# Kernel tuning notes

Measured on AMD Instinct MI355X. Metric: run time of the kernel, lower is better.

The kernel has to match this reference:

```python
import jax, jax.numpy as jnp
import numpy as np

SIZE = 11
SIGMA = 1.5
DEPTH = 1
C1 = (0.01 * DEPTH) ** 2
C2 = (0.03 * DEPTH) ** 2


def _fspecial_gauss(size, sigma):
    # mimics the MATLAB fspecial gaussian used by the torch module
    x, y = np.mgrid[-size // 2 + 1: size // 2 + 1, -size // 2 + 1: size // 2 + 1]
    g = np.exp(-((x ** 2 + y ** 2) / (2.0 * sigma ** 2)))
    g = g / g.sum()
    return jnp.asarray(g, dtype=jnp.float32)[None, None]  # [1,1,size,size]


def setup_inputs() -> dict:
    key = jax.random.key(0)
    k1, k2 = jax.random.split(key)
    N, C, H, W = 64, 1, 512, 512
    y_hat = jax.random.uniform(k1, (N, C, H, W), dtype=jnp.float32)
    y = jax.random.uniform(k2, (N, C, H, W), dtype=jnp.float32)
    window = _fspecial_gauss(SIZE, SIGMA)
    return {"y_hat": y_hat, "y": y, "window": window}


def _conv(x, w):
    # valid conv, stride 1, NCHW / OIHW
    return jax.lax.conv_general_dilated(
        x, w, window_strides=(1, 1), padding="VALID",
        dimension_numbers=("NCHW", "OIHW", "NCHW"))


def _ssim(y_hat, y, window):
    N = y_hat.shape[0]
    # single conv over the 5 stacked maps (y_hat, y, y_hat^2, y^2, y_hat*y)
    stacked = jnp.concatenate(
        [y_hat, y, y_hat * y_hat, y * y, y_hat * y], axis=0)
    conv = _conv(stacked, window)
    mu1, mu2, s11, s22, s12 = jnp.split(conv, 5, axis=0)
    mu1_sq = mu1 * mu1
    mu2_sq = mu2 * mu2
    mu1_mu2 = mu1 * mu2
    sigma1_sq = s11 - mu1_sq
    sigma2_sq = s22 - mu2_sq
    sigma12 = s12 - mu1_mu2
    score = ((2 * mu1_mu2 + C1) * (2 * sigma12 + C2)) / (
        (mu1_sq + mu2_sq + C1) * (sigma1_sq + sigma2_sq + C2))
    return jnp.mean(score)


def reference(y_hat, y, window):
    return _ssim(y_hat, y, window)
```

## Files before the change

kernel.cpp:

```cpp
#include <hip/hip_runtime.h>

#define KS 11
#define TBX 32
#define TBY 32
#define NROWS 42
#define HST 34
#define IMG 512
#define OUT_H 502
#define OUT_W 502
#define N_IMG 64
#define GXD 16
#define GYD 16
#define NBLK (GXD * GYD * N_IMG)

__global__ __launch_bounds__(256, 4) void ssim_main(
    const float* __restrict__ g_a, const float* __restrict__ g_b,
    const float* __restrict__ g_w, float* __restrict__ bsum)
{
  __shared__ float s_h[5][NROWS][HST];
  __shared__ float s_red[4];

  const int t = threadIdx.x;
  const int x0 = blockIdx.x * TBX, y0 = blockIdx.y * TBY;
  const float* __restrict__ A = g_a + (size_t)blockIdx.z * (IMG * IMG);
  const float* __restrict__ B = g_b + (size_t)blockIdx.z * (IMG * IMG);

  float u[KS];
  {
    const float inv = 1.0f / sqrtf(g_w[5 * KS + 5]);
#pragma unroll
    for (int j = 0; j < KS; ++j) u[j] = g_w[j * KS + 5] * inv;
  }

  const bool edge = (x0 == IMG - TBX) || (y0 == IMG - TBX);
  if (t < 252) {
    const int r = t / 6;
    const int k = t - r * 6;
    const int c0 = (k == 5) ? 26 : 6 * k;
    const int gy = y0 + r;
    const int gxs = x0 + c0;

    float ea[16], eb[16];
    if (!edge) {
      const float* pa = A + gy * IMG + gxs;
      const float* pb = B + gy * IMG + gxs;
#pragma unroll
      for (int i = 0; i < 8; ++i) {
        const float2 va = *(const float2*)(pa + 2 * i);
        const float2 vb = *(const float2*)(pb + 2 * i);
        ea[2 * i] = va.x; ea[2 * i + 1] = va.y;
        eb[2 * i] = vb.x; eb[2 * i + 1] = vb.y;
      }
    } else {
      const int gyc = min(gy, IMG - 1);
      const float* pa = A + gyc * IMG;
      const float* pb = B + gyc * IMG;
#pragma unroll
      for (int i = 0; i < 16; ++i) {
        const int gx = min(gxs + i, IMG - 1);
        ea[i] = pa[gx];
        eb[i] = pb[gx];
      }
    }

    float hm1[6], hm2[6], h11[6], h22[6], h12[6];
#pragma unroll
    for (int cc = 0; cc < 6; ++cc) {
      float m1 = 0.f, m2 = 0.f, q11 = 0.f, q22 = 0.f, q12 = 0.f;
#pragma unroll
      for (int j = 0; j < KS; ++j) {
        const float a = ea[cc + j], b = eb[cc + j];
        const float ta = u[j] * a, tb = u[j] * b;
        m1 += ta;
        m2 += tb;
        q11 = fmaf(ta, a, q11);
        q22 = fmaf(tb, b, q22);
        q12 = fmaf(ta, b, q12);
      }
      hm1[cc] = m1; hm2[cc] = m2; h11[cc] = q11; h22[cc] = q22; h12[cc] = q12;
    }

#define WRMAP(m, arr)                                                   \
    *(float2*)&s_h[m][r][c0]     = make_float2(arr[0], arr[1]);         \
    *(float2*)&s_h[m][r][c0 + 2] = make_float2(arr[2], arr[3]);         \
    *(float2*)&s_h[m][r][c0 + 4] = make_float2(arr[4], arr[5]);
    WRMAP(0, hm1) WRMAP(1, hm2) WRMAP(2, h11) WRMAP(3, h22) WRMAP(4, h12)
#undef WRMAP
  }
  __syncthreads();

  const int x = t & 31;
  const int yq = (t >> 5) << 2;
  float omu1[4], omu2[4], os11[4], os22[4], os12[4];

  auto vconv = [&](int m, float* o) {
    float v[14];
#pragma unroll
    for (int kk = 0; kk < 14; ++kk) v[kk] = s_h[m][yq + kk][x];
#pragma unroll
    for (int yy = 0; yy < 4; ++yy) {
      float a_ = 0.f;
#pragma unroll
      for (int i = 0; i < KS; ++i) a_ = fmaf(u[i], v[yy + i], a_);
      o[yy] = a_;
    }
  };
  vconv(0, omu1);
  vconv(1, omu2);
  vconv(2, os11);
  vconv(3, os22);
  vconv(4, os12);

  float score = 0.f;
  const int gx_ = x0 + x;
#pragma unroll
  for (int yy = 0; yy < 4; ++yy) {
    const int gy_ = y0 + yq + yy;
    if (gx_ < OUT_W && gy_ < OUT_H) {
      const float C1 = 1e-4f, C2 = 9e-4f;
      const float mu1 = omu1[yy], mu2 = omu2[yy];
      const float mu1s = mu1 * mu1, mu2s = mu2 * mu2, m12 = mu1 * mu2;
      const float sig1 = os11[yy] - mu1s, sig2 = os22[yy] - mu2s,
                  sig12 = os12[yy] - m12;
      score += ((2.f * m12 + C1) * (2.f * sig12 + C2)) /
               ((mu1s + mu2s + C1) * (sig1 + sig2 + C2));
    }
  }

#pragma unroll
  for (int off = 32; off > 0; off >>= 1)
    score += __shfl_down(score, off);
  const int wave = t >> 6, lane = t & 63;
  if (lane == 0) s_red[wave] = score;
  __syncthreads();
  if (t == 0) {
    const int bid = (int)((blockIdx.z * GYD + blockIdx.y) * GXD + blockIdx.x);
    bsum[bid] = s_red[0] + s_red[1] + s_red[2] + s_red[3];
  }
}

__global__ __launch_bounds__(256) void ssim_final(
    const float* __restrict__ bsum, float* __restrict__ out)
{
  double v = 0.0;
  for (int i = threadIdx.x; i < NBLK; i += 256) v += (double)bsum[i];
#pragma unroll
  for (int off = 32; off > 0; off >>= 1)
    v += __shfl_down(v, off);
  __shared__ double s_red[4];
  const int wave = (int)threadIdx.x >> 6, lane = (int)threadIdx.x & 63;
  if (lane == 0) s_red[wave] = v;
  __syncthreads();
  if (threadIdx.x == 0) {
    const double total = s_red[0] + s_red[1] + s_red[2] + s_red[3];
    out[0] = (float)(total / (double)((size_t)N_IMG * OUT_H * OUT_W));
  }
}

extern "C" void kernel_launch(void* const* d_in, const int* in_sizes, int n_in,
                              void* d_out, int out_size, void* d_ws, size_t ws_size,
                              hipStream_t stream) {
  const float* yh = (const float*)d_in[0];
  const float* yy = (const float*)d_in[1];
  const float* w  = (const float*)d_in[2];
  float* bsum = (float*)d_ws;
  float* out = (float*)d_out;

  dim3 grid(GXD, GYD, N_IMG);
  hipLaunchKernelGGL(ssim_main, grid, dim3(256), 0, stream, yh, yy, w, bsum);
  hipLaunchKernelGGL(ssim_final, dim3(1), dim3(256), 0, stream, bsum, out);
}
```

Before: 257.8 us.

## Use ring-buffered shared rows with two-phase separable SSIM to shrink LDS

Replaces the 42-row horizontal-pass buffer with a 32-slot ring buffer filled in two phases, so each block computes the first 16 output rows, refills 16 new rows and then computes the rest. This lowers LDS per block and raises the launch-bounds occupancy hint from 4 to 8 blocks. Horizontal tasks now cover 4 columns each with float4 loads, and the row stride changes to 35 to avoid bank conflicts. It adds an extra barrier pair and serialises two load/compute phases. The final reduction also reads the block sums with float4 loads.

```diff
diff --git a/kernel.cpp b/kernel.cpp
--- a/kernel.cpp
+++ b/kernel.cpp
@@ -3,8 +3,8 @@
 #define KS 11
 #define TBX 32
 #define TBY 32
-#define NROWS 42
-#define HST 34
+#define SLOTS 32
+#define HST 35
 #define IMG 512
 #define OUT_H 502
 #define OUT_W 502
@@ -12,18 +12,20 @@
 #define GXD 16
 #define GYD 16
 #define NBLK (GXD * GYD * N_IMG)
+#define MSTRIDE (SLOTS * HST)
 
-__global__ __launch_bounds__(256, 4) void ssim_main(
+__global__ __launch_bounds__(256, 8) void ssim_main(
     const float* __restrict__ g_a, const float* __restrict__ g_b,
     const float* __restrict__ g_w, float* __restrict__ bsum)
 {
-  __shared__ float s_h[5][NROWS][HST];
+  __shared__ float s_h[5 * MSTRIDE];
   __shared__ float s_red[4];
 
   const int t = threadIdx.x;
   const int x0 = blockIdx.x * TBX, y0 = blockIdx.y * TBY;
   const float* __restrict__ A = g_a + (size_t)blockIdx.z * (IMG * IMG);
   const float* __restrict__ B = g_b + (size_t)blockIdx.z * (IMG * IMG);
+  const bool edge = (x0 == IMG - TBX) || (y0 == IMG - TBX);
 
   float u[KS];
   {
@@ -32,40 +34,39 @@
     for (int j = 0; j < KS; ++j) u[j] = g_w[j * KS + 5] * inv;
   }
 
-  const bool edge = (x0 == IMG - TBX) || (y0 == IMG - TBX);
-  if (t < 252) {
-    const int r = t / 6;
-    const int k = t - r * 6;
-    const int c0 = (k == 5) ? 26 : 6 * k;
-    const int gy = y0 + r;
+  auto htask = [&](int r_abs, int k) {
+    const int c0 = 4 * k;
+    const int slot = r_abs & (SLOTS - 1);
+    const int gy = y0 + r_abs;
     const int gxs = x0 + c0;
 
-    float ea[16], eb[16];
+    float ea[14], eb[14];
     if (!edge) {
       const float* pa = A + gy * IMG + gxs;
       const float* pb = B + gy * IMG + gxs;
-#pragma unroll
-      for (int i = 0; i < 8; ++i) {
-        const float2 va = *(const float2*)(pa + 2 * i);
-        const float2 vb = *(const float2*)(pb + 2 * i);
-        ea[2 * i] = va.x; ea[2 * i + 1] = va.y;
-        eb[2 * i] = vb.x; eb[2 * i + 1] = vb.y;
-      }
+      *(float4*)&ea[0] = *(const float4*)(pa);
+      *(float4*)&ea[4] = *(const float4*)(pa + 4);
+      *(float4*)&ea[8] = *(const float4*)(pa + 8);
+      *(float2*)&ea[12] = *(const float2*)(pa + 12);
+      *(float4*)&eb[0] = *(const float4*)(pb);
+      *(float4*)&eb[4] = *(const float4*)(pb + 4);
+      *(float4*)&eb[8] = *(const float4*)(pb + 8);
+      *(float2*)&eb[12] = *(const float2*)(pb + 12);
     } else {
       const int gyc = min(gy, IMG - 1);
       const float* pa = A + gyc * IMG;
       const float* pb = B + gyc * IMG;
 #pragma unroll
-      for (int i = 0; i < 16; ++i) {
+      for (int i = 0; i < 14; ++i) {
         const int gx = min(gxs + i, IMG - 1);
         ea[i] = pa[gx];
         eb[i] = pb[gx];
       }
     }
 
-    float hm1[6], hm2[6], h11[6], h22[6], h12[6];
+    float* dst = &s_h[slot * HST + c0];
 #pragma unroll
-    for (int cc = 0; cc < 6; ++cc) {
+    for (int cc = 0; cc < 4; ++cc) {
       float m1 = 0.f, m2 = 0.f, q11 = 0.f, q22 = 0.f, q12 = 0.f;
 #pragma unroll
       for (int j = 0; j < KS; ++j) {
@@ -77,55 +78,64 @@
         q22 = fmaf(tb, b, q22);
         q12 = fmaf(ta, b, q12);
       }
-      hm1[cc] = m1; hm2[cc] = m2; h11[cc] = q11; h22[cc] = q22; h12[cc] = q12;
+      dst[0 * MSTRIDE + cc] = m1;
+      dst[1 * MSTRIDE + cc] = m2;
+      dst[2 * MSTRIDE + cc] = q11;
+      dst[3 * MSTRIDE + cc] = q22;
+      dst[4 * MSTRIDE + cc] = q12;
+    }
+  };
+
+  auto vtask = [&](int ybase_phase) -> float {
+    const int x = t & 31;
+    const int yb = ybase_phase + 2 * (t >> 5);
+    int addr[12];
+#pragma unroll
+    for (int k = 0; k < 12; ++k)
+      addr[k] = ((yb + k) & (SLOTS - 1)) * HST + x;
+
+    float o[5][2];
+#pragma unroll
+    for (int m = 0; m < 5; ++m) {
+      const float* base = &s_h[m * MSTRIDE];
+      float v[12];
+#pragma unroll
+      for (int k = 0; k < 12; ++k) v[k] = base[addr[k]];
+      float a0 = 0.f, a1 = 0.f;
+#pragma unroll
+      for (int i = 0; i < KS; ++i) {
+        a0 = fmaf(u[i], v[i], a0);
+        a1 = fmaf(u[i], v[i + 1], a1);
+      }
+      o[m][0] = a0;
+      o[m][1] = a1;
     }
 
-#define WRMAP(m, arr)                                                   \
-    *(float2*)&s_h[m][r][c0]     = make_float2(arr[0], arr[1]);         \
-    *(float2*)&s_h[m][r][c0 + 2] = make_float2(arr[2], arr[3]);         \
-    *(float2*)&s_h[m][r][c0 + 4] = make_float2(arr[4], arr[5]);
-    WRMAP(0, hm1) WRMAP(1, hm2) WRMAP(2, h11) WRMAP(3, h22) WRMAP(4, h12)
-#undef WRMAP
-  }
+    float sc = 0.f;
+    const int gx_ = x0 + x;
+#pragma unroll
+    for (int yy = 0; yy < 2; ++yy) {
+      const int gy_ = y0 + yb + yy;
+      if (gx_ < OUT_W && gy_ < OUT_H) {
+        const float C1 = 1e-4f, C2 = 9e-4f;
+        const float mu1 = o[0][yy], mu2 = o[1][yy];
+        const float mu1s = mu1 * mu1, mu2s = mu2 * mu2, m12 = mu1 * mu2;
+        const float sig1 = o[2][yy] - mu1s, sig2 = o[3][yy] - mu2s,
+                    sig12 = o[4][yy] - m12;
+        sc += ((2.f * m12 + C1) * (2.f * sig12 + C2)) /
+              ((mu1s + mu2s + C1) * (sig1 + sig2 + C2));
+      }
+    }
+    return sc;
+  };
+
+  if (t < 208) htask(t >> 3, t & 7);
   __syncthreads();
-
-  const int x = t & 31;
-  const int yq = (t >> 5) << 2;
-  float omu1[4], omu2[4], os11[4], os22[4], os12[4];
-
-  auto vconv = [&](int m, float* o) {
-    float v[14];
-#pragma unroll
-    for (int kk = 0; kk < 14; ++kk) v[kk] = s_h[m][yq + kk][x];
-#pragma unroll
-    for (int yy = 0; yy < 4; ++yy) {
-      float a_ = 0.f;
-#pragma unroll
-      for (int i = 0; i < KS; ++i) a_ = fmaf(u[i], v[yy + i], a_);
-      o[yy] = a_;
-    }
-  };
-  vconv(0, omu1);
-  vconv(1, omu2);
-  vconv(2, os11);
-  vconv(3, os22);
-  vconv(4, os12);
-
-  float score = 0.f;
-  const int gx_ = x0 + x;
-#pragma unroll
-  for (int yy = 0; yy < 4; ++yy) {
-    const int gy_ = y0 + yq + yy;
-    if (gx_ < OUT_W && gy_ < OUT_H) {
-      const float C1 = 1e-4f, C2 = 9e-4f;
-      const float mu1 = omu1[yy], mu2 = omu2[yy];
-      const float mu1s = mu1 * mu1, mu2s = mu2 * mu2, m12 = mu1 * mu2;
-      const float sig1 = os11[yy] - mu1s, sig2 = os22[yy] - mu2s,
-                  sig12 = os12[yy] - m12;
-      score += ((2.f * m12 + C1) * (2.f * sig12 + C2)) /
-               ((mu1s + mu2s + C1) * (sig1 + sig2 + C2));
-    }
-  }
+  float score = vtask(0);
+  __syncthreads();
+  if (t < 128) htask(26 + (t >> 3), t & 7);
+  __syncthreads();
+  score += vtask(16);
 
 #pragma unroll
   for (int off = 32; off > 0; off >>= 1)
@@ -142,8 +152,13 @@
 __global__ __launch_bounds__(256) void ssim_final(
     const float* __restrict__ bsum, float* __restrict__ out)
 {
+  const float4* b4 = (const float4*)bsum;
   double v = 0.0;
-  for (int i = threadIdx.x; i < NBLK; i += 256) v += (double)bsum[i];
+#pragma unroll
+  for (int k = 0; k < 16; ++k) {
+    const float4 f = b4[k * 256 + threadIdx.x];
+    v += (double)((f.x + f.y) + (f.z + f.w));
+  }
 #pragma unroll
   for (int off = 32; off > 0; off >>= 1)
     v += __shfl_down(v, off);
```

New measurement: 259.4 us. About the same (+0.6%).

## Stream rows per wave with register ring buffer instead of shared-memory tiles

Applied to the files above, without the earlier changes.

Replaces the two-phase shared-memory tile (horizontal pass to LDS, sync, vertical pass) with a per-wave column strip. Each lane walks 77 input rows, does an 11-tap horizontal pass on its own 12 loaded values and keeps the last 11 horizontal results per map in a register ring for the vertical pass. This removes LDS traffic, barriers and the halo recomputation between neighbouring tiles. In exchange, every lane reloads 12 overlapping floats per row and relies on the cache for reuse, and the grid shrinks to fewer, longer-running waves. The SSIM divide also becomes a hardware reciprocal, and the final reduction reads the per-wave sums with float4 loads.

```diff
diff --git a/kernel.cpp b/kernel.cpp
--- a/kernel.cpp
+++ b/kernel.cpp
@@ -1,159 +1,120 @@
 #include <hip/hip_runtime.h>
 
-#define KS 11
-#define TBX 32
-#define TBY 32
-#define NROWS 42
-#define HST 34
 #define IMG 512
-#define OUT_H 502
-#define OUT_W 502
+#define OUT_HW 502
 #define N_IMG 64
-#define GXD 16
-#define GYD 16
-#define NBLK (GXD * GYD * N_IMG)
+#define XT 8
+#define YT 8
+#define NWAVE (XT * YT * N_IMG)
 
 __global__ __launch_bounds__(256, 4) void ssim_main(
     const float* __restrict__ g_a, const float* __restrict__ g_b,
     const float* __restrict__ g_w, float* __restrict__ bsum)
 {
-  __shared__ float s_h[5][NROWS][HST];
-  __shared__ float s_red[4];
+  const int t = threadIdx.x;
+  const int lane = t & 63;
+  const int wv = t >> 6;
+  const int bx = blockIdx.x;
+  const int ty = ((int)blockIdx.y << 2) | wv;
+  const int y0 = ty << 6;
 
-  const int t = threadIdx.x;
-  const int x0 = blockIdx.x * TBX, y0 = blockIdx.y * TBY;
   const float* __restrict__ A = g_a + (size_t)blockIdx.z * (IMG * IMG);
   const float* __restrict__ B = g_b + (size_t)blockIdx.z * (IMG * IMG);
 
-  float u[KS];
+  const int x = (bx << 6) | lane;
+  const int xc = min(x, 500);
+  const bool off1 = (x >= 501);
+  const bool xvalid = (x <= 501);
+
+  float u[11], ue[12];
   {
-    const float inv = 1.0f / sqrtf(g_w[5 * KS + 5]);
+    const float inv = 1.0f / sqrtf(g_w[5 * 11 + 5]);
 #pragma unroll
-    for (int j = 0; j < KS; ++j) u[j] = g_w[j * KS + 5] * inv;
+    for (int j = 0; j < 11; ++j) u[j] = g_w[j * 11 + 5] * inv;
+    ue[0] = off1 ? 0.f : u[0];
+#pragma unroll
+    for (int j = 1; j < 11; ++j) ue[j] = off1 ? u[j - 1] : u[j];
+    ue[11] = off1 ? u[10] : 0.f;
   }
 
-  const bool edge = (x0 == IMG - TBX) || (y0 == IMG - TBX);
-  if (t < 252) {
-    const int r = t / 6;
-    const int k = t - r * 6;
-    const int c0 = (k == 5) ? 26 : 6 * k;
-    const int gy = y0 + r;
-    const int gxs = x0 + c0;
+  float win[5][11];
+  float score = 0.f;
 
-    float ea[16], eb[16];
-    if (!edge) {
-      const float* pa = A + gy * IMG + gxs;
-      const float* pb = B + gy * IMG + gxs;
+  for (int i = 0; i < 7; ++i) {
 #pragma unroll
-      for (int i = 0; i < 8; ++i) {
-        const float2 va = *(const float2*)(pa + 2 * i);
-        const float2 vb = *(const float2*)(pb + 2 * i);
-        ea[2 * i] = va.x; ea[2 * i + 1] = va.y;
-        eb[2 * i] = vb.x; eb[2 * i + 1] = vb.y;
+    for (int s = 0; s < 11; ++s) {
+      const int r = 11 * i + s;
+      const int gy = min(y0 + r, IMG - 1);
+      const float* pa = A + (gy << 9) + xc;
+      const float* pb = B + (gy << 9) + xc;
+      float a[12], b[12];
+      __builtin_memcpy(a, pa, 48);
+      __builtin_memcpy(b, pb, 48);
+
+      float h0 = 0.f, h1 = 0.f, h2 = 0.f, h3 = 0.f, h4 = 0.f;
+#pragma unroll
+      for (int j = 0; j < 12; ++j) {
+        const float ta = ue[j] * a[j], tb = ue[j] * b[j];
+        h0 += ta;
+        h1 += tb;
+        h2 = fmaf(ta, a[j], h2);
+        h3 = fmaf(tb, b[j], h3);
+        h4 = fmaf(ta, b[j], h4);
       }
-    } else {
-      const int gyc = min(gy, IMG - 1);
-      const float* pa = A + gyc * IMG;
-      const float* pb = B + gyc * IMG;
+      win[0][s] = h0; win[1][s] = h1; win[2][s] = h2;
+      win[3][s] = h3; win[4][s] = h4;
+
+      if (i > 0 || s == 10) {
+        float o[5];
 #pragma unroll
-      for (int i = 0; i < 16; ++i) {
-        const int gx = min(gxs + i, IMG - 1);
-        ea[i] = pa[gx];
-        eb[i] = pb[gx];
+        for (int m = 0; m < 5; ++m) {
+          float acc = 0.f;
+#pragma unroll
+          for (int k = 0; k < 11; ++k)
+            acc = fmaf(u[k], win[m][(s + 1 + k) % 11], acc);
+          o[m] = acc;
+        }
+        const int yo = y0 + r - 10;
+        const bool valid = xvalid && (yo <= OUT_HW - 1) && (r <= 73);
+        const float C1 = 1e-4f, C2 = 9e-4f;
+        const float mu1 = o[0], mu2 = o[1];
+        const float mu1s = mu1 * mu1, mu2s = mu2 * mu2, m12 = mu1 * mu2;
+        const float sig1 = o[2] - mu1s, sig2 = o[3] - mu2s, sig12 = o[4] - m12;
+        const float num = (2.f * m12 + C1) * (2.f * sig12 + C2);
+        const float den = (mu1s + mu2s + C1) * (sig1 + sig2 + C2);
+        const float val = num * __builtin_amdgcn_rcpf(den);
+        score += valid ? val : 0.f;
       }
-    }
-
-    float hm1[6], hm2[6], h11[6], h22[6], h12[6];
-#pragma unroll
-    for (int cc = 0; cc < 6; ++cc) {
-      float m1 = 0.f, m2 = 0.f, q11 = 0.f, q22 = 0.f, q12 = 0.f;
-#pragma unroll
-      for (int j = 0; j < KS; ++j) {
-        const float a = ea[cc + j], b = eb[cc + j];
-        const float ta = u[j] * a, tb = u[j] * b;
-        m1 += ta;
-        m2 += tb;
-        q11 = fmaf(ta, a, q11);
-        q22 = fmaf(tb, b, q22);
-        q12 = fmaf(ta, b, q12);
-      }
-      hm1[cc] = m1; hm2[cc] = m2; h11[cc] = q11; h22[cc] = q22; h12[cc] = q12;
-    }
-
-#define WRMAP(m, arr)                                                   \
-    *(float2*)&s_h[m][r][c0]     = make_float2(arr[0], arr[1]);         \
-    *(float2*)&s_h[m][r][c0 + 2] = make_float2(arr[2], arr[3]);         \
-    *(float2*)&s_h[m][r][c0 + 4] = make_float2(arr[4], arr[5]);
-    WRMAP(0, hm1) WRMAP(1, hm2) WRMAP(2, h11) WRMAP(3, h22) WRMAP(4, h12)
-#undef WRMAP
-  }
-  __syncthreads();
-
-  const int x = t & 31;
-  const int yq = (t >> 5) << 2;
-  float omu1[4], omu2[4], os11[4], os22[4], os12[4];
-
-  auto vconv = [&](int m, float* o) {
-    float v[14];
-#pragma unroll
-    for (int kk = 0; kk < 14; ++kk) v[kk] = s_h[m][yq + kk][x];
-#pragma unroll
-    for (int yy = 0; yy < 4; ++yy) {
-      float a_ = 0.f;
-#pragma unroll
-      for (int i = 0; i < KS; ++i) a_ = fmaf(u[i], v[yy + i], a_);
-      o[yy] = a_;
-    }
-  };
-  vconv(0, omu1);
-  vconv(1, omu2);
-  vconv(2, os11);
-  vconv(3, os22);
-  vconv(4, os12);
-
-  float score = 0.f;
-  const int gx_ = x0 + x;
-#pragma unroll
-  for (int yy = 0; yy < 4; ++yy) {
-    const int gy_ = y0 + yq + yy;
-    if (gx_ < OUT_W && gy_ < OUT_H) {
-      const float C1 = 1e-4f, C2 = 9e-4f;
-      const float mu1 = omu1[yy], mu2 = omu2[yy];
-      const float mu1s = mu1 * mu1, mu2s = mu2 * mu2, m12 = mu1 * mu2;
-      const float sig1 = os11[yy] - mu1s, sig2 = os22[yy] - mu2s,
-                  sig12 = os12[yy] - m12;
-      score += ((2.f * m12 + C1) * (2.f * sig12 + C2)) /
-               ((mu1s + mu2s + C1) * (sig1 + sig2 + C2));
     }
   }
 
 #pragma unroll
-  for (int off = 32; off > 0; off >>= 1)
-    score += __shfl_down(score, off);
-  const int wave = t >> 6, lane = t & 63;
-  if (lane == 0) s_red[wave] = score;
-  __syncthreads();
-  if (t == 0) {
-    const int bid = (int)((blockIdx.z * GYD + blockIdx.y) * GXD + blockIdx.x);
-    bsum[bid] = s_red[0] + s_red[1] + s_red[2] + s_red[3];
+  for (int o = 32; o > 0; o >>= 1) score += __shfl_down(score, o);
+  if (lane == 0) {
+    const int widx = ((int)blockIdx.z * YT + ty) * XT + bx;
+    bsum[widx] = score;
   }
 }
 
 __global__ __launch_bounds__(256) void ssim_final(
     const float* __restrict__ bsum, float* __restrict__ out)
 {
+  const float4* b4 = (const float4*)bsum;
   double v = 0.0;
-  for (int i = threadIdx.x; i < NBLK; i += 256) v += (double)bsum[i];
 #pragma unroll
-  for (int off = 32; off > 0; off >>= 1)
-    v += __shfl_down(v, off);
+  for (int k = 0; k < 4; ++k) {
+    const float4 f = b4[k * 256 + threadIdx.x];
+    v += (double)((f.x + f.y) + (f.z + f.w));
+  }
+#pragma unroll
+  for (int off = 32; off > 0; off >>= 1) v += __shfl_down(v, off);
   __shared__ double s_red[4];
   const int wave = (int)threadIdx.x >> 6, lane = (int)threadIdx.x & 63;
   if (lane == 0) s_red[wave] = v;
   __syncthreads();
   if (threadIdx.x == 0) {
     const double total = s_red[0] + s_red[1] + s_red[2] + s_red[3];
-    out[0] = (float)(total / (double)((size_t)N_IMG * OUT_H * OUT_W));
+    out[0] = (float)(total / (double)((size_t)N_IMG * OUT_HW * OUT_HW));
   }
 }
 
@@ -166,7 +127,7 @@
   float* bsum = (float*)d_ws;
   float* out = (float*)d_out;
 
-  dim3 grid(GXD, GYD, N_IMG);
+  dim3 grid(XT, YT / 4, N_IMG);
   hipLaunchKernelGGL(ssim_main, grid, dim3(256), 0, stream, yh, yy, w, bsum);
   hipLaunchKernelGGL(ssim_final, dim3(1), dim3(256), 0, stream, bsum, out);
 }
```

Result: slower. 454.6 us (+76.3%).
